# Kernel tuning notes

Hardware: AMD Instinct MI355X
Metric: run time of the kernel (lower is better)

Reference implementation:

```python
import jax, jax.numpy as jnp
import numpy as np


def _sage_conv(x, edge_index, W_l, b, W_r, num_nodes):
    # PyG SAGEConv (mean aggr): out = lin_l(mean_{src in N(dst)} x[src]) + lin_r(x)
    src, dst = edge_index[0], edge_index[1]
    msg = x[src]                                                   # [E, d]
    agg = jax.ops.segment_sum(msg, dst, num_segments=num_nodes)    # [N, d]
    deg = jax.ops.segment_sum(jnp.ones((edge_index.shape[1],), x.dtype), dst,
                              num_segments=num_nodes)              # [N]
    agg = agg / jnp.maximum(deg, 1.0)[:, None]
    return agg @ W_l.T + b + x @ W_r.T


def setup_inputs() -> dict:
    key = jax.random.key(0)
    ks = jax.random.split(key, 8)
    N, J, I, E1, E2, D = 50000, 25000, 12500, 600000, 300000, 128
    s = 1.0 / np.sqrt(D)
    return {
        "feat": jax.random.normal(ks[0], (N, D), dtype=jnp.float32),
        "t_adj": jax.random.randint(ks[1], (2, E1), 0, N, dtype=jnp.int64),
        "n_adj": jax.random.randint(ks[2], (2, E2), 0, J, dtype=jnp.int64),
        "i": I,
        "j": J,
        "W1_l": jax.random.normal(ks[3], (D, D), dtype=jnp.float32) * s,
        "b1": jnp.zeros((D,), dtype=jnp.float32),
        "W1_r": jax.random.normal(ks[4], (D, D), dtype=jnp.float32) * s,
        "W2_l": jax.random.normal(ks[5], (D, D), dtype=jnp.float32) * s,
        "b2": jnp.zeros((D,), dtype=jnp.float32),
        "W2_r": jax.random.normal(ks[6], (D, D), dtype=jnp.float32) * s,
    }


def reference(feat, t_adj, n_adj, i, j, W1_l, b1, W1_r, W2_l, b2, W2_r):
    N = feat.shape[0]
    x1 = _sage_conv(feat, t_adj, W1_l, b1, W1_r, N)[:j]
    x1 = jax.nn.relu(x1)
    # F.dropout(p=0.5, training=True): fixed mask key for determinism
    keep = jax.random.bernoulli(jax.random.key(1), 0.5, x1.shape)
    x1 = jnp.where(keep, x1 * 2.0, 0.0)
    x2 = _sage_conv(x1, n_adj, W2_l, b2, W2_r, j)[:i]
    return x2
```

## Files before the change

### kernel.cpp

```cpp
#include <hip/hip_runtime.h>
#include <stdint.h>

#define DD 128
#define NJ 25000
#define NI 12500

__device__ __forceinline__ uint32_t rotl32(uint32_t v, int n) {
  return (v << n) | (v >> (32 - n));
}

__device__ __forceinline__ void threefry_0_1(uint32_t& x0, uint32_t& x1) {
  const uint32_t ks0 = 0u, ks1 = 1u, ks2 = 0x1BD11BDBu;
  x0 += ks0; x1 += ks1;
#define TF_R4(a,b,c,d)                                  \
  x0 += x1; x1 = rotl32(x1,(a)); x1 ^= x0;              \
  x0 += x1; x1 = rotl32(x1,(b)); x1 ^= x0;              \
  x0 += x1; x1 = rotl32(x1,(c)); x1 ^= x0;              \
  x0 += x1; x1 = rotl32(x1,(d)); x1 ^= x0;
  TF_R4(13,15,26,6)   x0 += ks1; x1 += ks2 + 1u;
  TF_R4(17,29,16,24)  x0 += ks2; x1 += ks0 + 2u;
  TF_R4(13,15,26,6)   x0 += ks0; x1 += ks1 + 3u;
  TF_R4(17,29,16,24)  x0 += ks1; x1 += ks2 + 4u;
  TF_R4(13,15,26,6)   x0 += ks2; x1 += ks0 + 5u;
#undef TF_R4
}

__device__ __forceinline__ bool dropout_keep(uint32_t f) {
  uint32_t x0 = 0u, x1 = f;
  threefry_0_1(x0, x1);
  return ((x0 ^ x1) >> 31) == 0u;
}

__device__ __forceinline__ float4 ld4(const float* p) {
  return *(const float4*)p;
}

__device__ __forceinline__ int detect_flag_block(const int* __restrict__ w,
                                                 int* sf) {
  if (threadIdx.x == 0) {
    int is64 = 1;
    for (int e = 0; e < 16; ++e)
      if (w[2 * e + 1] != 0) is64 = 0;
    *sf = is64;
  }
  __syncthreads();
  return *sf;
}

__global__ void setup_hist(const float* __restrict__ Wl1,
                           const float* __restrict__ Wr1,
                           float* __restrict__ WT1,
                           const float* __restrict__ Wl2,
                           const float* __restrict__ Wr2,
                           float* __restrict__ WT2,
                           const int* __restrict__ adj1,
                           const int* __restrict__ adj2,
                           int* __restrict__ cnt1, int* __restrict__ cnt2,
                           int nE1, int nE2) {
  const int b = blockIdx.x;
  if (b < 256) {
    int t = b * 256 + threadIdx.x;
    int which = t >= DD * 256;
    int idx = which ? t - DD * 256 : t;
    const float* Wl = which ? Wl2 : Wl1;
    const float* Wr = which ? Wr2 : Wr1;
    float* WTp = which ? WT2 : WT1;
    int c = idx >> 8;
    int k = idx & 255;
    float v = (k < DD) ? Wl[c * DD + k] : Wr[c * DD + (k - DD)];
    WTp[(k >> 2) * (DD * 4) + c * 4 + (k & 3)] = v;
    return;
  }
  __shared__ int sf;
  const int f = detect_flag_block(adj1, &sf);
  int t = (b - 256) * 256 + threadIdx.x;
  if (t < nE1) {
    int d = f ? adj1[2 * nE1 + 2 * t] : adj1[nE1 + t];
    if (d < NJ) atomicAdd(&cnt1[d], 1);
  } else if (t < nE1 + nE2) {
    int e = t - nE1;
    int d = f ? adj2[2 * nE2 + 2 * e] : adj2[nE2 + e];
    if (d < NI) atomicAdd(&cnt2[d], 1);
  }
}

__global__ void scan2(int* __restrict__ a1, int n1, int* __restrict__ a2,
                      int n2) {
  __shared__ int part[1024];
  int* a = blockIdx.x ? a2 : a1;
  const int n = blockIdx.x ? n2 : n1;
  const int t = threadIdx.x;
  const int per = (n + 1023) / 1024;
  int lo = t * per;
  int hi = lo + per;
  if (hi > n) hi = n;
  int sum = 0;
  for (int i = lo; i < hi; ++i) sum += a[i];
  part[t] = sum;
  __syncthreads();
  for (int ofs = 1; ofs < 1024; ofs <<= 1) {
    int v = (t >= ofs) ? part[t - ofs] : 0;
    __syncthreads();
    part[t] += v;
    __syncthreads();
  }
  int run = (t == 0) ? 0 : part[t - 1];
  for (int i = lo; i < hi; ++i) {
    int v = a[i];
    a[i] = run;
    run += v;
  }
}

__global__ void fill_both(const int* __restrict__ adj1,
                          const int* __restrict__ adj2,
                          int* __restrict__ cur1, int* __restrict__ cur2,
                          int* __restrict__ csr1, int* __restrict__ csr2,
                          int nE1, int nE2) {
  __shared__ int sf;
  const int f = detect_flag_block(adj1, &sf);
  int t = blockIdx.x * blockDim.x + threadIdx.x;
  if (t < nE1) {
    int s, d;
    if (f) {
      s = adj1[2 * t];
      d = adj1[2 * nE1 + 2 * t];
    } else {
      s = adj1[t];
      d = adj1[nE1 + t];
    }
    if (d < NJ) csr1[atomicAdd(&cur1[d], 1)] = s;
  } else if (t < nE1 + nE2) {
    int e = t - nE1;
    int s, d;
    if (f) {
      s = adj2[2 * e];
      d = adj2[2 * nE2 + 2 * e];
    } else {
      s = adj2[e];
      d = adj2[nE2 + e];
    }
    if (d < NI) csr2[atomicAdd(&cur2[d], 1)] = s;
  }
}

template <int ROWS, int LAYER>
__global__ __launch_bounds__(256) void dense_kernel(
    const float* __restrict__ xsrc, const int* __restrict__ csr,
    const int* __restrict__ offEnd, const float* __restrict__ xin,
    const float* __restrict__ WTp, const float* __restrict__ bias,
    float* __restrict__ out, int M) {
  __shared__ float As[ROWS * 256];
  const int tid = threadIdx.x;
  const int rowBase = blockIdx.x * ROWS;
  constexpr int RPT = ROWS / 8;

  {
    const int team = tid >> 5;
    const int l4 = (tid & 31) * 4;
#pragma unroll
    for (int rr = 0; rr < RPT; ++rr) {
      const int r = team * RPT + rr;
      int rg = rowBase + r;
      if (rg >= M) rg = M - 1;
      const int end = offEnd[rg];
      const int start = (rg == 0) ? 0 : offEnd[rg - 1];
      float4 a0 = {0.f, 0.f, 0.f, 0.f}, a1 = a0, a2 = a0, a3 = a0;
      int e = start;
      for (; e + 7 < end; e += 8) {
        int s0 = csr[e], s1 = csr[e + 1], s2 = csr[e + 2], s3 = csr[e + 3];
        int s4 = csr[e + 4], s5 = csr[e + 5], s6 = csr[e + 6], s7 = csr[e + 7];
        float4 v0 = ld4(xsrc + (size_t)s0 * DD + l4);
        float4 v1 = ld4(xsrc + (size_t)s1 * DD + l4);
        float4 v2 = ld4(xsrc + (size_t)s2 * DD + l4);
        float4 v3 = ld4(xsrc + (size_t)s3 * DD + l4);
        float4 v4 = ld4(xsrc + (size_t)s4 * DD + l4);
        float4 v5 = ld4(xsrc + (size_t)s5 * DD + l4);
        float4 v6 = ld4(xsrc + (size_t)s6 * DD + l4);
        float4 v7 = ld4(xsrc + (size_t)s7 * DD + l4);
        a0.x += v0.x; a0.y += v0.y; a0.z += v0.z; a0.w += v0.w;
        a1.x += v1.x; a1.y += v1.y; a1.z += v1.z; a1.w += v1.w;
        a2.x += v2.x; a2.y += v2.y; a2.z += v2.z; a2.w += v2.w;
        a3.x += v3.x; a3.y += v3.y; a3.z += v3.z; a3.w += v3.w;
        a0.x += v4.x; a0.y += v4.y; a0.z += v4.z; a0.w += v4.w;
        a1.x += v5.x; a1.y += v5.y; a1.z += v5.z; a1.w += v5.w;
        a2.x += v6.x; a2.y += v6.y; a2.z += v6.z; a2.w += v6.w;
        a3.x += v7.x; a3.y += v7.y; a3.z += v7.z; a3.w += v7.w;
      }
      for (; e + 3 < end; e += 4) {
        int s0 = csr[e], s1 = csr[e + 1], s2 = csr[e + 2], s3 = csr[e + 3];
        float4 v0 = ld4(xsrc + (size_t)s0 * DD + l4);
        float4 v1 = ld4(xsrc + (size_t)s1 * DD + l4);
        float4 v2 = ld4(xsrc + (size_t)s2 * DD + l4);
        float4 v3 = ld4(xsrc + (size_t)s3 * DD + l4);
        a0.x += v0.x; a0.y += v0.y; a0.z += v0.z; a0.w += v0.w;
        a1.x += v1.x; a1.y += v1.y; a1.z += v1.z; a1.w += v1.w;
        a2.x += v2.x; a2.y += v2.y; a2.z += v2.z; a2.w += v2.w;
        a3.x += v3.x; a3.y += v3.y; a3.z += v3.z; a3.w += v3.w;
      }
      for (; e < end; ++e) {
        float4 v = ld4(xsrc + (size_t)csr[e] * DD + l4);
        a0.x += v.x; a0.y += v.y; a0.z += v.z; a0.w += v.w;
      }
      a0.x += a1.x + a2.x + a3.x;
      a0.y += a1.y + a2.y + a3.y;
      a0.z += a1.z + a2.z + a3.z;
      a0.w += a1.w + a2.w + a3.w;
      float rdeg = 1.0f / fmaxf((float)(end - start), 1.0f);
      a0.x *= rdeg; a0.y *= rdeg; a0.z *= rdeg; a0.w *= rdeg;
      *(float4*)(As + r * 256 + l4) = a0;
      *(float4*)(As + r * 256 + DD + l4) = ld4(xin + (size_t)rg * DD + l4);
    }
  }
  __syncthreads();

  const int u = tid & 31;
  const int g = tid >> 5;
  const int r0 = g * RPT;
  float acc[RPT][4];
#pragma unroll
  for (int r = 0; r < RPT; ++r)
    acc[r][0] = acc[r][1] = acc[r][2] = acc[r][3] = 0.f;

#pragma unroll 8
  for (int k0 = 0; k0 < 256; k0 += 4) {
    const float* wbase = WTp + (k0 >> 2) * (DD * 4);
    float4 w0 = ld4(wbase + u * 4);
    float4 w1 = ld4(wbase + (u + 32) * 4);
    float4 w2 = ld4(wbase + (u + 64) * 4);
    float4 w3 = ld4(wbase + (u + 96) * 4);
#pragma unroll
    for (int r = 0; r < RPT; ++r) {
      float4 a = *(const float4*)(As + (r0 + r) * 256 + k0);
      acc[r][0] += a.x * w0.x + a.y * w0.y + a.z * w0.z + a.w * w0.w;
      acc[r][1] += a.x * w1.x + a.y * w1.y + a.z * w1.z + a.w * w1.w;
      acc[r][2] += a.x * w2.x + a.y * w2.y + a.z * w2.z + a.w * w2.w;
      acc[r][3] += a.x * w3.x + a.y * w3.y + a.z * w3.z + a.w * w3.w;
    }
  }

  float bb[4] = {bias[u], bias[u + 32], bias[u + 64], bias[u + 96]};
#pragma unroll
  for (int r = 0; r < RPT; ++r) {
    int rg = rowBase + r0 + r;
    if (rg >= M) continue;
#pragma unroll
    for (int i = 0; i < 4; ++i) {
      int cc = u + 32 * i;
      float v = acc[r][i] + bb[i];
      if (LAYER == 1) {
        v = fmaxf(v, 0.0f);
        v = dropout_keep((uint32_t)rg * DD + (uint32_t)cc) ? v * 2.0f : 0.0f;
      }
      out[(size_t)rg * DD + cc] = v;
    }
  }
}

extern "C" void kernel_launch(void* const* d_in, const int* in_sizes, int n_in,
                              void* d_out, int out_size, void* d_ws, size_t ws_size,
                              hipStream_t stream) {
  const float* feat = (const float*)d_in[0];
  const int* t_adj = (const int*)d_in[1];
  const int* n_adj = (const int*)d_in[2];
  const float* W1l = (const float*)d_in[5];
  const float* b1 = (const float*)d_in[6];
  const float* W1r = (const float*)d_in[7];
  const float* W2l = (const float*)d_in[8];
  const float* b2 = (const float*)d_in[9];
  const float* W2r = (const float*)d_in[10];

  const int E1 = in_sizes[1] / 2;
  const int E2 = in_sizes[2] / 2;

  float* ws = (float*)d_ws;
  float* x1 = ws;
  float* WT1 = x1 + 3200000;
  float* WT2 = WT1 + 32768;
  int* off1 = (int*)(WT2 + 32768);
  int* off2 = off1 + NJ;
  int* csr1 = off2 + NI;
  int* csr2 = csr1 + E1;

  hipMemsetAsync(off1, 0, (size_t)(NJ + NI) * sizeof(int), stream);

  const int nTot = E1 + E2;
  const int histBlocks = (nTot + 255) / 256;
  setup_hist<<<256 + histBlocks, 256, 0, stream>>>(
      W1l, W1r, WT1, W2l, W2r, WT2, t_adj, n_adj, off1, off2, E1, E2);

  scan2<<<2, 1024, 0, stream>>>(off1, NJ, off2, NI);

  fill_both<<<(nTot + 255) / 256, 256, 0, stream>>>(t_adj, n_adj, off1, off2,
                                                    csr1, csr2, E1, E2);

  dense_kernel<32, 1><<<(NJ + 31) / 32, 256, 0, stream>>>(
      feat, csr1, off1, feat, WT1, b1, x1, NJ);
  dense_kernel<16, 2><<<(NI + 15) / 16, 256, 0, stream>>>(
      x1, csr2, off2, x1, WT2, b2, (float*)d_out, NI);
}
```

Measured before the change: 284.6 us.

## Replace CSR build with fixed-capacity per-node buckets and overflow list

Replaces the histogram, scan and fill kernels with a single pass that scatters each edge's source into a fixed-capacity bucket per destination node. Edges beyond the capacity go to a global overflow list that the aggregation kernel scans linearly. This drops two kernel launches and the single-block serial scan. In exchange it adds workspace pressure and a slow fallback for high-degree nodes. Aggregation order within a bucket is nondeterministic.

```diff
diff --git a/kernel.cpp b/kernel.cpp
--- a/kernel.cpp
+++ b/kernel.cpp
@@ -4,6 +4,7 @@
 #define DD 128
 #define NJ 25000
 #define NI 12500
+#define OVCAP 65536
 
 __device__ __forceinline__ uint32_t rotl32(uint32_t v, int n) {
   return (v << n) | (v >> (32 - n));
@@ -47,16 +48,21 @@
   return *sf;
 }
 
-__global__ void setup_hist(const float* __restrict__ Wl1,
-                           const float* __restrict__ Wr1,
-                           float* __restrict__ WT1,
-                           const float* __restrict__ Wl2,
-                           const float* __restrict__ Wr2,
-                           float* __restrict__ WT2,
-                           const int* __restrict__ adj1,
-                           const int* __restrict__ adj2,
-                           int* __restrict__ cnt1, int* __restrict__ cnt2,
-                           int nE1, int nE2) {
+__global__ void setup_bucket(const float* __restrict__ Wl1,
+                             const float* __restrict__ Wr1,
+                             float* __restrict__ WT1,
+                             const float* __restrict__ Wl2,
+                             const float* __restrict__ Wr2,
+                             float* __restrict__ WT2,
+                             const int* __restrict__ adj1,
+                             const int* __restrict__ adj2,
+                             int* __restrict__ cnt1, int* __restrict__ cnt2,
+                             int* __restrict__ ovCnt,
+                             int* __restrict__ ovList1,
+                             int* __restrict__ ovList2,
+                             int* __restrict__ bucket1,
+                             int* __restrict__ bucket2,
+                             int nE1, int nE2, int CAP) {
   const int b = blockIdx.x;
   if (b < 256) {
     int t = b * 256 + threadIdx.x;
@@ -75,52 +81,6 @@
   const int f = detect_flag_block(adj1, &sf);
   int t = (b - 256) * 256 + threadIdx.x;
   if (t < nE1) {
-    int d = f ? adj1[2 * nE1 + 2 * t] : adj1[nE1 + t];
-    if (d < NJ) atomicAdd(&cnt1[d], 1);
-  } else if (t < nE1 + nE2) {
-    int e = t - nE1;
-    int d = f ? adj2[2 * nE2 + 2 * e] : adj2[nE2 + e];
-    if (d < NI) atomicAdd(&cnt2[d], 1);
-  }
-}
-
-__global__ void scan2(int* __restrict__ a1, int n1, int* __restrict__ a2,
-                      int n2) {
-  __shared__ int part[1024];
-  int* a = blockIdx.x ? a2 : a1;
-  const int n = blockIdx.x ? n2 : n1;
-  const int t = threadIdx.x;
-  const int per = (n + 1023) / 1024;
-  int lo = t * per;
-  int hi = lo + per;
-  if (hi > n) hi = n;
-  int sum = 0;
-  for (int i = lo; i < hi; ++i) sum += a[i];
-  part[t] = sum;
-  __syncthreads();
-  for (int ofs = 1; ofs < 1024; ofs <<= 1) {
-    int v = (t >= ofs) ? part[t - ofs] : 0;
-    __syncthreads();
-    part[t] += v;
-    __syncthreads();
-  }
-  int run = (t == 0) ? 0 : part[t - 1];
-  for (int i = lo; i < hi; ++i) {
-    int v = a[i];
-    a[i] = run;
-    run += v;
-  }
-}
-
-__global__ void fill_both(const int* __restrict__ adj1,
-                          const int* __restrict__ adj2,
-                          int* __restrict__ cur1, int* __restrict__ cur2,
-                          int* __restrict__ csr1, int* __restrict__ csr2,
-                          int nE1, int nE2) {
-  __shared__ int sf;
-  const int f = detect_flag_block(adj1, &sf);
-  int t = blockIdx.x * blockDim.x + threadIdx.x;
-  if (t < nE1) {
     int s, d;
     if (f) {
       s = adj1[2 * t];
@@ -129,7 +89,15 @@
       s = adj1[t];
       d = adj1[nE1 + t];
     }
-    if (d < NJ) csr1[atomicAdd(&cur1[d], 1)] = s;
+    if (d < NJ) {
+      int pos = atomicAdd(&cnt1[d], 1);
+      if (pos < CAP) {
+        bucket1[(size_t)d * CAP + pos] = s;
+      } else {
+        int op = atomicAdd(&ovCnt[0], 1);
+        if (op < OVCAP) { ovList1[2 * op] = d; ovList1[2 * op + 1] = s; }
+      }
+    }
   } else if (t < nE1 + nE2) {
     int e = t - nE1;
     int s, d;
@@ -140,16 +108,25 @@
       s = adj2[e];
       d = adj2[nE2 + e];
     }
-    if (d < NI) csr2[atomicAdd(&cur2[d], 1)] = s;
+    if (d < NI) {
+      int pos = atomicAdd(&cnt2[d], 1);
+      if (pos < CAP) {
+        bucket2[(size_t)d * CAP + pos] = s;
+      } else {
+        int op = atomicAdd(&ovCnt[1], 1);
+        if (op < OVCAP) { ovList2[2 * op] = d; ovList2[2 * op + 1] = s; }
+      }
+    }
   }
 }
 
 template <int ROWS, int LAYER>
 __global__ __launch_bounds__(256) void dense_kernel(
-    const float* __restrict__ xsrc, const int* __restrict__ csr,
-    const int* __restrict__ offEnd, const float* __restrict__ xin,
+    const float* __restrict__ xsrc, const int* __restrict__ bucket,
+    const int* __restrict__ cnt, const int* __restrict__ ovCnt,
+    const int* __restrict__ ovList, const float* __restrict__ xin,
     const float* __restrict__ WTp, const float* __restrict__ bias,
-    float* __restrict__ out, int M) {
+    float* __restrict__ out, int M, int CAP) {
   __shared__ float As[ROWS * 256];
   const int tid = threadIdx.x;
   const int rowBase = blockIdx.x * ROWS;
@@ -163,13 +140,14 @@
       const int r = team * RPT + rr;
       int rg = rowBase + r;
       if (rg >= M) rg = M - 1;
-      const int end = offEnd[rg];
-      const int start = (rg == 0) ? 0 : offEnd[rg - 1];
+      const int deg = cnt[rg];
+      const int nb = (deg < CAP) ? deg : CAP;
+      const int* bk = bucket + (size_t)rg * CAP;
       float4 a0 = {0.f, 0.f, 0.f, 0.f}, a1 = a0, a2 = a0, a3 = a0;
-      int e = start;
-      for (; e + 7 < end; e += 8) {
-        int s0 = csr[e], s1 = csr[e + 1], s2 = csr[e + 2], s3 = csr[e + 3];
-        int s4 = csr[e + 4], s5 = csr[e + 5], s6 = csr[e + 6], s7 = csr[e + 7];
+      int e = 0;
+      for (; e + 7 < nb; e += 8) {
+        int s0 = bk[e], s1 = bk[e + 1], s2 = bk[e + 2], s3 = bk[e + 3];
+        int s4 = bk[e + 4], s5 = bk[e + 5], s6 = bk[e + 6], s7 = bk[e + 7];
         float4 v0 = ld4(xsrc + (size_t)s0 * DD + l4);
         float4 v1 = ld4(xsrc + (size_t)s1 * DD + l4);
         float4 v2 = ld4(xsrc + (size_t)s2 * DD + l4);
@@ -187,8 +165,8 @@
         a2.x += v6.x; a2.y += v6.y; a2.z += v6.z; a2.w += v6.w;
         a3.x += v7.x; a3.y += v7.y; a3.z += v7.z; a3.w += v7.w;
       }
-      for (; e + 3 < end; e += 4) {
-        int s0 = csr[e], s1 = csr[e + 1], s2 = csr[e + 2], s3 = csr[e + 3];
+      for (; e + 3 < nb; e += 4) {
+        int s0 = bk[e], s1 = bk[e + 1], s2 = bk[e + 2], s3 = bk[e + 3];
         float4 v0 = ld4(xsrc + (size_t)s0 * DD + l4);
         float4 v1 = ld4(xsrc + (size_t)s1 * DD + l4);
         float4 v2 = ld4(xsrc + (size_t)s2 * DD + l4);
@@ -198,15 +176,25 @@
         a2.x += v2.x; a2.y += v2.y; a2.z += v2.z; a2.w += v2.w;
         a3.x += v3.x; a3.y += v3.y; a3.z += v3.z; a3.w += v3.w;
       }
-      for (; e < end; ++e) {
-        float4 v = ld4(xsrc + (size_t)csr[e] * DD + l4);
+      for (; e < nb; ++e) {
+        float4 v = ld4(xsrc + (size_t)bk[e] * DD + l4);
         a0.x += v.x; a0.y += v.y; a0.z += v.z; a0.w += v.w;
+      }
+      if (deg > CAP) {
+        int ovc = *ovCnt;
+        if (ovc > OVCAP) ovc = OVCAP;
+        for (int o = 0; o < ovc; ++o) {
+          if (ovList[2 * o] == rg) {
+            float4 v = ld4(xsrc + (size_t)ovList[2 * o + 1] * DD + l4);
+            a0.x += v.x; a0.y += v.y; a0.z += v.z; a0.w += v.w;
+          }
+        }
       }
       a0.x += a1.x + a2.x + a3.x;
       a0.y += a1.y + a2.y + a3.y;
       a0.z += a1.z + a2.z + a3.z;
       a0.w += a1.w + a2.w + a3.w;
-      float rdeg = 1.0f / fmaxf((float)(end - start), 1.0f);
+      float rdeg = 1.0f / fmaxf((float)deg, 1.0f);
       a0.x *= rdeg; a0.y *= rdeg; a0.z *= rdeg; a0.w *= rdeg;
       *(float4*)(As + r * 256 + l4) = a0;
       *(float4*)(As + r * 256 + DD + l4) = ld4(xin + (size_t)rg * DD + l4);
@@ -277,25 +265,31 @@
   float* x1 = ws;
   float* WT1 = x1 + 3200000;
   float* WT2 = WT1 + 32768;
-  int* off1 = (int*)(WT2 + 32768);
-  int* off2 = off1 + NJ;
-  int* csr1 = off2 + NI;
-  int* csr2 = csr1 + E1;
-
-  hipMemsetAsync(off1, 0, (size_t)(NJ + NI) * sizeof(int), stream);
+  int* cnt1 = (int*)(WT2 + 32768);
+  int* cnt2 = cnt1 + NJ;
+  int* ovCnt = cnt2 + NI;
+  int* ovList1 = ovCnt + 8;
+  int* ovList2 = ovList1 + 2 * OVCAP;
+  int* bucket1 = ovList2 + 2 * OVCAP;
+
+  const long fixedInts = 3200000L + 32768 + 32768 + NJ + NI + 8 + 4L * OVCAP;
+  long capInts = (long)(ws_size / 4) - fixedInts;
+  int CAP = (int)(capInts / (NJ + NI));
+  if (CAP > 64) CAP = 64;
+  if (CAP < 16) CAP = 16;
+
+  int* bucket2 = bucket1 + (size_t)NJ * CAP;
+
+  hipMemsetAsync(cnt1, 0, (size_t)(NJ + NI + 8) * sizeof(int), stream);
 
   const int nTot = E1 + E2;
-  const int histBlocks = (nTot + 255) / 256;
-  setup_hist<<<256 + histBlocks, 256, 0, stream>>>(
-      W1l, W1r, WT1, W2l, W2r, WT2, t_adj, n_adj, off1, off2, E1, E2);
-
-  scan2<<<2, 1024, 0, stream>>>(off1, NJ, off2, NI);
-
-  fill_both<<<(nTot + 255) / 256, 256, 0, stream>>>(t_adj, n_adj, off1, off2,
-                                                    csr1, csr2, E1, E2);
+  setup_bucket<<<256 + (nTot + 255) / 256, 256, 0, stream>>>(
+      W1l, W1r, WT1, W2l, W2r, WT2, t_adj, n_adj, cnt1, cnt2, ovCnt, ovList1,
+      ovList2, bucket1, bucket2, E1, E2, CAP);
 
   dense_kernel<32, 1><<<(NJ + 31) / 32, 256, 0, stream>>>(
-      feat, csr1, off1, feat, WT1, b1, x1, NJ);
+      feat, bucket1, cnt1, ovCnt + 0, ovList1, feat, WT1, b1, x1, NJ, CAP);
   dense_kernel<16, 2><<<(NI + 15) / 16, 256, 0, stream>>>(
-      x1, csr2, off2, x1, WT2, b2, (float*)d_out, NI);
-}
+      x1, bucket2, cnt2, ovCnt + 1, ovList2, x1, WT2, b2, (float*)d_out, NI,
+      CAP);
+}
```

Measured after the change: 228.6 us. -19.7%, faster.
